# Optimization experiments

Measured on AMD Instinct MI355X. Metric: run time of the kernel, lower is better.

## Reference

```python
import jax, jax.numpy as jnp
import numpy as np

K_NN = 9  # kernel_size: neighbors per node (includes self, dist 0)


def knn_edges(feat):
    """feat: (B, C, N). Replicates DenseDilatedKnnGraph (dilation=1):
    L2-normalize over channels, dense pairwise sq-distance, top-k nearest."""
    nrm = jnp.sqrt(jnp.sum(feat * feat, axis=1, keepdims=True))
    xn = feat / jnp.maximum(nrm, 1e-12)            # F.normalize(dim=1)
    xt = jnp.swapaxes(xn, 1, 2)                    # (B, N, C)
    sq = jnp.sum(xt * xt, axis=-1)                 # (B, N)
    dist = sq[:, :, None] + sq[:, None, :] - 2.0 * jnp.einsum('bnc,bmc->bnm', xt, xt)
    _, nn_idx = jax.lax.top_k(-dist, K_NN)         # (B, N, k)
    center = jnp.broadcast_to(jnp.arange(nn_idx.shape[1], dtype=nn_idx.dtype)[None, :, None], nn_idx.shape)
    return nn_idx, center                          # (x_j sources, x_i targets)


def reference(x, W0, W1, bias):
    B, C, H, W = x.shape
    N = H * W
    NB = B * N
    feat = x.reshape(B, C, N)
    # KNN graph is built on detached features in the torch source
    x_j, x_i = knn_edges(jax.lax.stop_gradient(feat))
    E = B * N * K_NN
    # faithful to source: torch.linspace(0, B, steps=E, dtype=int64) batch offsets
    count = jnp.linspace(0.0, float(B), E).astype(jnp.int32)
    src = x_j.reshape(-1).astype(jnp.int32) + count * N
    dst = x_i.reshape(-1).astype(jnp.int32) + count * N
    valid = (src < NB) & (dst < NB)                # drop the out-of-range tail edge
    # flat_nodes: (B, C, H, W) -> (B*H*W, C), node id = b*HW + pixel
    nodes = jnp.swapaxes(feat, 1, 2).reshape(NB, C)
    # ChebConv K=2, sym norm, lambda_max=2: Tx0 = x, Tx1 = -(D^-1/2 A D^-1/2) x
    w = valid.astype(nodes.dtype)
    deg = jax.ops.segment_sum(w, src, num_segments=NB)
    dinv = jnp.where(deg > 0, jax.lax.rsqrt(jnp.maximum(deg, 1.0)), 0.0)
    norm = -(dinv[src] * w * dinv[dst])            # scaled-Laplacian edge weights
    msg = norm[:, None] * nodes[src]               # (E, C) gather + weight
    Tx1 = jax.ops.segment_sum(msg, dst, num_segments=NB)
    return nodes @ W0 + Tx1 @ W1 + bias


def setup_inputs() -> dict:
    key = jax.random.key(0)
    k1, k2, k3, k4 = jax.random.split(key, 4)
    B, C, H, W = 8, 48, 64, 64
    Cout = 48
    s = 1.0 / np.sqrt(C)
    return {
        'x': jax.random.normal(k1, (B, C, H, W), dtype=jnp.float32),
        'W0': jax.random.normal(k2, (C, Cout), dtype=jnp.float32) * s,
        'W1': jax.random.normal(k3, (C, Cout), dtype=jnp.float32) * s,
        'bias': jax.random.normal(k4, (Cout,), dtype=jnp.float32) * 0.01,
    }
```

## Files before the change

### kernel.cpp

```cpp
#include <hip/hip_runtime.h>

#define BATCH 8
#define CH    48
#define NPTS  4096
#define NBN   (BATCH*NPTS)
#define KNN   9
#define NCAND 12

typedef unsigned short u16;
typedef unsigned int   u32;
typedef unsigned long long u64;
typedef __bf16 bf16x8 __attribute__((ext_vector_type(8)));
typedef float  f32x4  __attribute__((ext_vector_type(4)));

__device__ __forceinline__ float bf2f(u16 v) { return __uint_as_float(((u32)v) << 16); }
__device__ __forceinline__ u16 f2bf(float f) {
  u32 u = __float_as_uint(f);
  u = (u + 0x7fffu + ((u >> 16) & 1u)) >> 16;
  return (u16)u;
}

#define MED3U(d, a, b, c) \
  asm("v_med3_u32 %0, %1, %2, %3" : "=v"(d) : "v"(a), "v"(b), "v"(c))
#define INS12(p0,p1,p2,p3,p4,p5,p6,p7,p8,p9,p10,p11,x) do { \
  MED3U(p11,p10,p11,x); MED3U(p10,p9,p10,x); MED3U(p9,p8,p9,x);  \
  MED3U(p8, p7, p8, x); MED3U(p7, p6,p7, x); MED3U(p6,p5,p6,x);  \
  MED3U(p5, p4, p5, x); MED3U(p4, p3,p4, x); MED3U(p3,p2,p3,x);  \
  MED3U(p2, p1, p2, x); MED3U(p1, p0,p1, x); p0 = min(p0, x);    \
} while (0)

__global__ __launch_bounds__(256)
void k_prep(const float* __restrict__ x, float* __restrict__ xraw,
            float* __restrict__ xn, float* __restrict__ csq,
            u16* __restrict__ Abuf, u16* __restrict__ Bbuf,
            int* __restrict__ deg) {
  int node = blockIdx.x * 256 + threadIdx.x;
  deg[node] = 0;
  int b = node >> 12, n = node & (NPTS - 1);
  const float* xb = x + (size_t)b * CH * NPTS;
  float f[CH];
#pragma unroll
  for (int c = 0; c < CH; ++c) f[c] = xb[(size_t)c * NPTS + n];
  float a0 = 0, a1 = 0, a2 = 0, a3 = 0;
#pragma unroll
  for (int k = 0; k < CH; k += 4) {
    a0 += f[k] * f[k]; a1 += f[k+1] * f[k+1];
    a2 += f[k+2] * f[k+2]; a3 += f[k+3] * f[k+3];
  }
  float nrm = fmaxf(sqrtf((a0 + a1) + (a2 + a3)), 1e-12f);
  float xv[CH];
#pragma unroll
  for (int c = 0; c < CH; ++c) xv[c] = f[c] / nrm;
  a0 = a1 = a2 = a3 = 0;
#pragma unroll
  for (int k = 0; k < CH; k += 4) {
    a0 += xv[k] * xv[k]; a1 += xv[k+1] * xv[k+1];
    a2 += xv[k+2] * xv[k+2]; a3 += xv[k+3] * xv[k+3];
  }
  float csqv = (a0 + a1) + (a2 + a3);
  csq[node] = csqv;
  float4* ro = (float4*)(xraw + (size_t)node * CH);
  float4* no = (float4*)(xn   + (size_t)node * CH);
#pragma unroll
  for (int i = 0; i < CH / 4; ++i) {
    ro[i] = make_float4(f[4*i], f[4*i+1], f[4*i+2], f[4*i+3]);
    no[i] = make_float4(xv[4*i], xv[4*i+1], xv[4*i+2], xv[4*i+3]);
  }
  u16 ah[64], al[64];
#pragma unroll
  for (int k = 0; k < CH; ++k) {
    float av = -2.0f * xv[k];
    u16 h = f2bf(av); ah[k] = h; al[k] = f2bf(av - bf2f(h));
  }
  { u16 h = f2bf(csqv); ah[48] = h; al[48] = f2bf(csqv - bf2f(h)); }
#pragma unroll
  for (int k = 49; k < 64; ++k) { ah[k] = 0; al[k] = 0; }
  u16* Bh = Bbuf + (size_t)node * 128;
#pragma unroll
  for (int k = 0; k < CH; ++k) {
    float bv = xv[k];
    u16 h = f2bf(bv); Bh[k] = h; Bh[64 + k] = f2bf(bv - bf2f(h));
  }
  Bh[48] = 0x3F80; Bh[64 + 48] = 0;
#pragma unroll
  for (int k = 49; k < 64; ++k) { Bh[k] = 0; Bh[64 + k] = 0; }
  u16* Ag = Abuf + (size_t)(node >> 4) * 2048 + (size_t)(node & 15) * 8;
#pragma unroll
  for (int v = 0; v < 4; ++v) {
    const u16* src = (v < 2) ? ah : al;
    int koff = (v & 1) * 32;
#pragma unroll
    for (int q = 0; q < 4; ++q) {
      uint4 pk;
      const u16* s = src + koff + q * 8;
      pk.x = (u32)s[0] | ((u32)s[1] << 16);
      pk.y = (u32)s[2] | ((u32)s[3] << 16);
      pk.z = (u32)s[4] | ((u32)s[5] << 16);
      pk.w = (u32)s[6] | ((u32)s[7] << 16);
      *(uint4*)(Ag + v * 512 + q * 128) = pk;
    }
  }
}

__global__ __launch_bounds__(256, 4)
void k_knn_m(const u16* __restrict__ Abuf, const u16* __restrict__ Bbuf,
             u32* __restrict__ candu) {
  int tid = threadIdx.x;
  int lane = tid & 63;
  int quad = lane >> 4, m16 = lane & 15;
  int panel = blockIdx.x * 4 + (tid >> 6);
  int row = panel * 16 + m16;
  int b4096 = row & ~(NPTS - 1);
  int quarter = blockIdx.y;
  int ct0 = quarter * 64;

  const __bf16* Bb = (const __bf16*)Bbuf + (size_t)row * 128;
  bf16x8 bh0 = *(const bf16x8*)(Bb + quad * 8);
  bf16x8 bh1 = *(const bf16x8*)(Bb + 32 + quad * 8);
  bf16x8 bl0 = *(const bf16x8*)(Bb + 64 + quad * 8);
  bf16x8 bl1 = *(const bf16x8*)(Bb + 96 + quad * 8);

  const __bf16* Ag = (const __bf16*)Abuf + (size_t)(b4096 >> 4) * 2048
                     + (size_t)lane * 8 + (size_t)ct0 * 2048;

  u32 s0=~0u,s1=~0u,s2=~0u,s3=~0u,s4=~0u,s5=~0u,
      s6=~0u,s7=~0u,s8=~0u,s9=~0u,s10=~0u,s11=~0u;

#define TILE_BODY(A0,A1,A2,A3,CT) do {                                      \
    f32x4 acc = {2.5f, 2.5f, 2.5f, 2.5f};                                   \
    acc = __builtin_amdgcn_mfma_f32_16x16x32_bf16(A0, bh0, acc, 0, 0, 0);   \
    acc = __builtin_amdgcn_mfma_f32_16x16x32_bf16(A1, bh1, acc, 0, 0, 0);   \
    acc = __builtin_amdgcn_mfma_f32_16x16x32_bf16(A0, bl0, acc, 0, 0, 0);   \
    acc = __builtin_amdgcn_mfma_f32_16x16x32_bf16(A1, bl1, acc, 0, 0, 0);   \
    acc = __builtin_amdgcn_mfma_f32_16x16x32_bf16(A2, bh0, acc, 0, 0, 0);   \
    acc = __builtin_amdgcn_mfma_f32_16x16x32_bf16(A3, bh1, acc, 0, 0, 0);   \
    u32 colb = ((u32)(CT) << 4) | ((u32)quad << 2);                         \
    _Pragma("unroll")                                                       \
    for (int r = 0; r < 4; ++r) {                                           \
      u32 u = __float_as_uint(acc[r]);                                      \
      u32 xx = (u & 0xFFFFF000u) | (colb | (u32)r);                         \
      INS12(s0,s1,s2,s3,s4,s5,s6,s7,s8,s9,s10,s11, xx);                     \
    }                                                                       \
  } while (0)

  bf16x8 a0 = *(const bf16x8*)(Ag);
  bf16x8 a1 = *(const bf16x8*)(Ag + 512);
  bf16x8 a2 = *(const bf16x8*)(Ag + 1024);
  bf16x8 a3 = *(const bf16x8*)(Ag + 1536);

  for (int t = 0; t < 64; t += 2) {
    const __bf16* apc = Ag + (size_t)(t + 1) * 2048;
    bf16x8 c0 = *(const bf16x8*)(apc);
    bf16x8 c1 = *(const bf16x8*)(apc + 512);
    bf16x8 c2 = *(const bf16x8*)(apc + 1024);
    bf16x8 c3 = *(const bf16x8*)(apc + 1536);

    TILE_BODY(a0, a1, a2, a3, ct0 + t);

    const __bf16* apn = Ag + (size_t)((t + 2 < 64) ? (t + 2) : 63) * 2048;
    a0 = *(const bf16x8*)(apn);
    a1 = *(const bf16x8*)(apn + 512);
    a2 = *(const bf16x8*)(apn + 1024);
    a3 = *(const bf16x8*)(apn + 1536);

    TILE_BODY(c0, c1, c2, c3, ct0 + t + 1);
  }
#undef TILE_BODY

  u32* o = candu + (((size_t)row * 4 + quarter) * 4 + quad) * NCAND;
  o[0]=s0; o[1]=s1; o[2]=s2; o[3]=s3; o[4]=s4; o[5]=s5;
  o[6]=s6; o[7]=s7; o[8]=s8; o[9]=s9; o[10]=s10; o[11]=s11;
}

__global__ __launch_bounds__(256, 4)
void k_reduce(const u32* __restrict__ candu, u32* __restrict__ cand12) {
  __shared__ u32 ls[64 * 4 * NCAND];
  int tid = threadIdx.x;
  int lr = tid >> 2, q = tid & 3;
  int row = blockIdx.x * 64 + lr;
  const u32* src = candu + (size_t)row * 192 + q * 48;
  u32 t0=~0u,t1=~0u,t2=~0u,t3=~0u,t4=~0u,t5=~0u,
      t6=~0u,t7=~0u,t8=~0u,t9=~0u,t10=~0u,t11=~0u;
  for (int s = 0; s < 48; ++s) {
    u32 x = src[s];
    INS12(t0,t1,t2,t3,t4,t5,t6,t7,t8,t9,t10,t11, x);
  }
  u32* lw = ls + (size_t)(lr * 4 + q) * NCAND;
  lw[0]=t0; lw[1]=t1; lw[2]=t2; lw[3]=t3; lw[4]=t4; lw[5]=t5;
  lw[6]=t6; lw[7]=t7; lw[8]=t8; lw[9]=t9; lw[10]=t10; lw[11]=t11;
  __syncthreads();
  if (q == 0) {
    u32 g0=~0u,g1=~0u,g2=~0u,g3=~0u,g4=~0u,g5=~0u,
        g6=~0u,g7=~0u,g8=~0u,g9=~0u,g10=~0u,g11=~0u;
    const u32* lsrc = ls + (size_t)lr * 48;
    for (int s = 0; s < 48; ++s) {
      u32 x = lsrc[s];
      INS12(g0,g1,g2,g3,g4,g5,g6,g7,g8,g9,g10,g11, x);
    }
    u32* o = cand12 + (size_t)row * NCAND;
    o[0]=(g0&0xFFFu); o[1]=(g1&0xFFFu); o[2]=(g2&0xFFFu);
    o[3]=(g3&0xFFFu); o[4]=(g4&0xFFFu); o[5]=(g5&0xFFFu);
    o[6]=(g6&0xFFFu); o[7]=(g7&0xFFFu); o[8]=(g8&0xFFFu);
    o[9]=(g9&0xFFFu); o[10]=(g10&0xFFFu); o[11]=(g11&0xFFFu);
  }
}

#define RR 16
__global__ __launch_bounds__(256, 4)
void k_rescore(const float* __restrict__ xn, const float* __restrict__ csq,
               const u32* __restrict__ cand12,
               u16* __restrict__ nn, int* __restrict__ deg) {
  __shared__ float dS[RR * NCAND];
  __shared__ int   iS[RR * NCAND];
  int tid = threadIdx.x;
  int lr = tid >> 4, q = tid & 15;
  int bi = blockIdx.x;
  int row = (bi & 7) * NPTS + (bi >> 3) * RR + lr;
  int b4096 = row & ~(NPTS - 1);
  const float* xnb = xn + (size_t)b4096 * CH;
  if (q < NCAND) {
    float rf[CH];
    const float4* p = (const float4*)(xn + (size_t)row * CH);
#pragma unroll
    for (int i = 0; i < CH / 4; ++i) {
      float4 v = p[i];
      rf[4*i] = v.x; rf[4*i+1] = v.y; rf[4*i+2] = v.z; rf[4*i+3] = v.w;
    }
    float sqn = csq[row];
    int c = (int)(cand12[(size_t)row * NCAND + q] & (NPTS - 1));
    const float4* cp = (const float4*)(xnb + (size_t)c * CH);
    float a0 = 0, a1 = 0, a2 = 0, a3 = 0;
#pragma unroll
    for (int i = 0; i < CH / 4; ++i) {
      float4 v = cp[i];
      a0 += rf[4*i]   * v.x; a1 += rf[4*i+1] * v.y;
      a2 += rf[4*i+2] * v.z; a3 += rf[4*i+3] * v.w;
    }
    float dist = (sqn + csq[b4096 + c]) - 2.0f * ((a0 + a1) + (a2 + a3));
    dS[lr * NCAND + q] = dist;
    iS[lr * NCAND + q] = c;
  }
  __syncthreads();
  if (q == 0) {
    float gd[KNN]; int gi[KNN];
#pragma unroll
    for (int j = 0; j < KNN; ++j) { gd[j] = 3.4e38f; gi[j] = 0x7fffffff; }
    for (int s = 0; s < NCAND; ++s) {
      float dc = dS[lr * NCAND + s]; int ic = iS[lr * NCAND + s];
      if (dc < gd[KNN - 1] || (dc == gd[KNN - 1] && ic < gi[KNN - 1])) {
        gd[KNN - 1] = dc; gi[KNN - 1] = ic;
#pragma unroll
        for (int k2 = KNN - 1; k2 > 0; --k2) {
          bool sw = (gd[k2] < gd[k2 - 1]) ||
                    (gd[k2] == gd[k2 - 1] && gi[k2] < gi[k2 - 1]);
          if (sw) {
            float td = gd[k2]; gd[k2] = gd[k2 - 1]; gd[k2 - 1] = td;
            int ti = gi[k2]; gi[k2] = gi[k2 - 1]; gi[k2 - 1] = ti;
          }
        }
      }
    }
    u16* o = nn + (size_t)row * KNN;
    int jmax = (row == NBN - 1) ? (KNN - 1) : KNN;
#pragma unroll
    for (int j = 0; j < KNN; ++j) o[j] = (u16)(gi[j] & (NPTS - 1));
    for (int j = 0; j < jmax; ++j)
      atomicAdd(&deg[b4096 + (gi[j] & (NPTS - 1))], 1);
  }
}

#define ONB 64
#define LPAD 52
__global__ __launch_bounds__(256)
void k_out_f(const float* __restrict__ xraw, const u16* __restrict__ nn,
             const int* __restrict__ deg,
             const float* __restrict__ W0, const float* __restrict__ W1,
             const float* __restrict__ bias, float* __restrict__ out) {
  __shared__ float w0[CH * CH], w1[CH * CH], bs[CH];
  __shared__ __align__(16) float fS[ONB * LPAD];
  __shared__ __align__(16) float txS[ONB * LPAD];
  __shared__ float dinvS[ONB];
  int tid = threadIdx.x;
  int bi = blockIdx.x;
  int n0 = (bi & 7) * NPTS + (bi >> 3) * ONB;
  int b12 = n0 & ~(NPTS - 1);
  for (int i = tid; i < CH * CH; i += 256) { w0[i] = W0[i]; w1[i] = W1[i]; }
  if (tid < CH) bs[tid] = bias[tid];
  for (int i = tid; i < ONB * 12; i += 256) {
    int ln = i / 12, f4 = i % 12;
    *(float4*)(fS + ln * LPAD + f4 * 4) =
        *(const float4*)(xraw + (size_t)(n0 + ln) * CH + f4 * 4);
  }
  if (tid < ONB) {
    int dg = deg[n0 + tid];
    dinvS[tid] = (dg > 0) ? (1.0f / sqrtf((float)dg)) : 0.0f;
  }
  __syncthreads();

  int ln = tid >> 2, p = tid & 3;
  int node = n0 + ln;
  float dn = dinvS[ln];
  const u16* nrow = nn + (size_t)node * KNN;
  bool full = (node != NBN - 1);
  float tx[12];
#pragma unroll
  for (int i = 0; i < 12; ++i) tx[i] = 0.f;
#pragma unroll
  for (int j = 0; j < KNN; ++j) {
    if (j < KNN - 1 || full) {
      int s = nrow[j] & (NPTS - 1);
      int dgs = deg[b12 + s];
      float ds = (dgs > 0) ? (1.0f / sqrtf((float)dgs)) : 0.0f;
      float w = -(ds * dn);
      const float4* pr = (const float4*)(xraw + (size_t)(b12 + s) * CH + p * 12);
#pragma unroll
      for (int q3 = 0; q3 < 3; ++q3) {
        float4 v = pr[q3];
        tx[q3*4]   += w * v.x; tx[q3*4+1] += w * v.y;
        tx[q3*4+2] += w * v.z; tx[q3*4+3] += w * v.w;
      }
    }
  }
#pragma unroll
  for (int q3 = 0; q3 < 3; ++q3)
    *(float4*)(txS + ln * LPAD + p * 12 + q3 * 4) =
        make_float4(tx[q3*4], tx[q3*4+1], tx[q3*4+2], tx[q3*4+3]);
  __syncthreads();

  float acc[12];
#pragma unroll
  for (int i = 0; i < 12; ++i) acc[i] = bs[p * 12 + i];
  const float* fr = fS + ln * LPAD;
  const float* tr = txS + ln * LPAD;
#pragma unroll
  for (int c = 0; c < CH; ++c) {
    float fc = fr[c];
    const float* wr = w0 + c * CH + p * 12;
#pragma unroll
    for (int i = 0; i < 12; ++i) acc[i] += fc * wr[i];
  }
#pragma unroll
  for (int c = 0; c < CH; ++c) {
    float tc = tr[c];
    const float* wr = w1 + c * CH + p * 12;
#pragma unroll
    for (int i = 0; i < 12; ++i) acc[i] += tc * wr[i];
  }
  float* op = out + (size_t)node * CH + p * 12;
#pragma unroll
  for (int q3 = 0; q3 < 3; ++q3)
    *(float4*)(op + q3 * 4) =
        make_float4(acc[q3*4], acc[q3*4+1], acc[q3*4+2], acc[q3*4+3]);
}

__global__ __launch_bounds__(256)
void k_zero(int* __restrict__ deg) { deg[blockIdx.x * 256 + threadIdx.x] = 0; }

__global__ __launch_bounds__(256)
void k_hist(const u16* __restrict__ nn, int* __restrict__ deg) {
  int node = blockIdx.x * 256 + threadIdx.x;
  int b12 = node & ~(NPTS - 1);
  int jmax = (node == NBN - 1) ? (KNN - 1) : KNN;
  for (int j = 0; j < jmax; ++j)
    atomicAdd(&deg[b12 + (nn[(size_t)node * KNN + j] & (NPTS - 1))], 1);
}

__global__ __launch_bounds__(256)
void k_dinv(const int* __restrict__ deg, float* __restrict__ dinv) {
  int i = blockIdx.x * 256 + threadIdx.x;
  int dg = deg[i];
  dinv[i] = (dg > 0) ? (1.0f / sqrtf((float)dg)) : 0.0f;
}

#define NQ    4
#define QCOLS (NPTS/NQ)
#define TCOLS 32
#define NTILES (QCOLS/TCOLS)
#define RPB   64

__global__ __launch_bounds__(256)
void k_knn_nb(const float* __restrict__ x, u16* __restrict__ nn) {
  __shared__ __align__(16) float tile[NQ * TCOLS * CH];
  __shared__ float nrmS[NQ * TCOLS];
  __shared__ float csq[NQ * TCOLS];
  int tid = threadIdx.x;
  int r0 = blockIdx.x * RPB;
  int b  = r0 >> 12;
  int q  = tid >> 6;
  int lr = tid & 63;
  int n  = (r0 + lr) & (NPTS - 1);
  const float* xb = x + (size_t)b * CH * NPTS;
  float rf[CH];
#pragma unroll
  for (int c = 0; c < CH; ++c) rf[c] = xb[(size_t)c * NPTS + n];
  float sqn;
  {
    float a0 = 0, a1 = 0, a2 = 0, a3 = 0;
#pragma unroll
    for (int k = 0; k < CH; k += 4) {
      a0 += rf[k] * rf[k]; a1 += rf[k+1] * rf[k+1];
      a2 += rf[k+2] * rf[k+2]; a3 += rf[k+3] * rf[k+3];
    }
    float nrm = fmaxf(sqrtf((a0 + a1) + (a2 + a3)), 1e-12f);
#pragma unroll
    for (int c = 0; c < CH; ++c) rf[c] = rf[c] / nrm;
    a0 = a1 = a2 = a3 = 0;
#pragma unroll
    for (int k = 0; k < CH; k += 4) {
      a0 += rf[k] * rf[k]; a1 += rf[k+1] * rf[k+1];
      a2 += rf[k+2] * rf[k+2]; a3 += rf[k+3] * rf[k+3];
    }
    sqn = (a0 + a1) + (a2 + a3);
  }
  float d[KNN]; int id[KNN];
#pragma unroll
  for (int j = 0; j < KNN; ++j) { d[j] = 3.4e38f; id[j] = 0x7fffffff; }
  for (int t = 0; t < NTILES; ++t) {
    __syncthreads();
#pragma unroll
    for (int qq = 0; qq < NQ; ++qq) {
      int colbase = qq * QCOLS + t * TCOLS;
      float* dst = tile + qq * TCOLS * CH;
#pragma unroll
      for (int it = 0; it < 6; ++it) {
        int i = it * 256 + tid;
        int c = i >> 5, p = i & 31;
        dst[p * CH + c] = xb[(size_t)c * NPTS + colbase + p];
      }
    }
    __syncthreads();
    if (tid < NQ * TCOLS) {
      const float* cp = tile + tid * CH;
      float a0 = 0, a1 = 0, a2 = 0, a3 = 0;
#pragma unroll
      for (int k = 0; k < CH; k += 4) {
        float4 v = *(const float4*)(cp + k);
        a0 += v.x * v.x; a1 += v.y * v.y; a2 += v.z * v.z; a3 += v.w * v.w;
      }
      nrmS[tid] = fmaxf(sqrtf((a0 + a1) + (a2 + a3)), 1e-12f);
    }
    __syncthreads();
    for (int i = tid; i < NQ * TCOLS * CH; i += 256)
      tile[i] = tile[i] / nrmS[i / CH];
    __syncthreads();
    if (tid < NQ * TCOLS) {
      const float* cp = tile + tid * CH;
      float a0 = 0, a1 = 0, a2 = 0, a3 = 0;
#pragma unroll
      for (int k = 0; k < CH; k += 4) {
        float4 v = *(const float4*)(cp + k);
        a0 += v.x * v.x; a1 += v.y * v.y; a2 += v.z * v.z; a3 += v.w * v.w;
      }
      csq[tid] = (a0 + a1) + (a2 + a3);
    }
    __syncthreads();
    int cbase = q * QCOLS + t * TCOLS;
    const float* tq = tile + q * TCOLS * CH;
    for (int cc = 0; cc < TCOLS; ++cc) {
      const float* cp = tq + cc * CH;
      float a0 = 0, a1 = 0, a2 = 0, a3 = 0;
#pragma unroll
      for (int k = 0; k < CH; k += 4) {
        float4 v = *(const float4*)(cp + k);
        a0 += rf[k] * v.x; a1 += rf[k+1] * v.y;
        a2 += rf[k+2] * v.z; a3 += rf[k+3] * v.w;
      }
      float dist = (sqn + csq[q * TCOLS + cc]) - 2.0f * ((a0 + a1) + (a2 + a3));
      if (dist < d[KNN - 1]) {
        d[KNN - 1] = dist; id[KNN - 1] = cbase + cc;
#pragma unroll
        for (int k2 = KNN - 1; k2 > 0; --k2) {
          if (d[k2] < d[k2 - 1]) {
            float td = d[k2]; d[k2] = d[k2 - 1]; d[k2 - 1] = td;
            int ti = id[k2]; id[k2] = id[k2 - 1]; id[k2 - 1] = ti;
          }
        }
      }
    }
  }
  __syncthreads();
  float* md = tile;
  int*   mi = (int*)(tile + 256 * KNN);
#pragma unroll
  for (int j = 0; j < KNN; ++j) { md[tid * KNN + j] = d[j]; mi[tid * KNN + j] = id[j]; }
  __syncthreads();
  if (tid < RPB) {
    float fd[KNN]; int fi[KNN];
#pragma unroll
    for (int j = 0; j < KNN; ++j) { fd[j] = 3.4e38f; fi[j] = 0x7fffffff; }
    for (int qq = 0; qq < NQ; ++qq) {
      int s = qq * RPB + tid;
      for (int j = 0; j < KNN; ++j) {
        float dc = md[s * KNN + j]; int ic = mi[s * KNN + j];
        if (dc < fd[KNN - 1]) {
          fd[KNN - 1] = dc; fi[KNN - 1] = ic;
#pragma unroll
          for (int k2 = KNN - 1; k2 > 0; --k2) {
            if (fd[k2] < fd[k2 - 1]) {
              float td = fd[k2]; fd[k2] = fd[k2 - 1]; fd[k2 - 1] = td;
              int ti = fi[k2]; fi[k2] = fi[k2 - 1]; fi[k2 - 1] = ti;
            }
          }
        }
      }
    }
    u16* o = nn + (size_t)(r0 + tid) * KNN;
#pragma unroll
    for (int j = 0; j < KNN; ++j) o[j] = (u16)(fi[j] & (NPTS - 1));
  }
}

__global__ __launch_bounds__(256)
void k_out_nb(const float* __restrict__ x, const u16* __restrict__ nn,
              const float* __restrict__ dinv,
              const float* __restrict__ W0, const float* __restrict__ W1,
              const float* __restrict__ bias, float* __restrict__ out) {
  __shared__ float w0[CH * CH], w1[CH * CH], bs[CH];
  for (int i = threadIdx.x; i < CH * CH; i += 256) { w0[i] = W0[i]; w1[i] = W1[i]; }
  if (threadIdx.x < CH) bs[threadIdx.x] = bias[threadIdx.x];
  __syncthreads();
  int node = blockIdx.x * 256 + threadIdx.x;
  int b = node >> 12, n = node & (NPTS - 1);
  const float* xb = x + (size_t)b * CH * NPTS;
  float f[CH], acc[CH], tx[CH];
#pragma unroll
  for (int c = 0; c < CH; ++c) f[c] = xb[(size_t)c * NPTS + n];
#pragma unroll
  for (int o = 0; o < CH; ++o) acc[o] = bs[o];
#pragma unroll
  for (int c = 0; c < CH; ++c) {
    float fc = f[c];
    const float* wr = w0 + c * CH;
#pragma unroll
    for (int o = 0; o < CH; ++o) acc[o] += fc * wr[o];
  }
#pragma unroll
  for (int c = 0; c < CH; ++c) tx[c] = 0.f;
  float dn = dinv[node];
  int jmax = (node == NBN - 1) ? (KNN - 1) : KNN;
  for (int j = 0; j < jmax; ++j) {
    int s = nn[(size_t)node * KNN + j] & (NPTS - 1);
    float w = -(dinv[(b << 12) + s] * dn);
#pragma unroll
    for (int c = 0; c < CH; ++c) tx[c] += w * xb[(size_t)c * NPTS + s];
  }
#pragma unroll
  for (int c = 0; c < CH; ++c) {
    float tc = tx[c];
    const float* wr = w1 + c * CH;
#pragma unroll
    for (int o = 0; o < CH; ++o) acc[o] += tc * wr[o];
  }
  float4* op = (float4*)(out + (size_t)node * CH);
#pragma unroll
  for (int i = 0; i < CH / 4; ++i)
    op[i] = make_float4(acc[4*i], acc[4*i+1], acc[4*i+2], acc[4*i+3]);
}

extern "C" void kernel_launch(void* const* d_in, const int* in_sizes, int n_in,
                              void* d_out, int out_size, void* d_ws, size_t ws_size,
                              hipStream_t stream) {
  const float* x    = (const float*)d_in[0];
  const float* W0   = (const float*)d_in[1];
  const float* W1   = (const float*)d_in[2];
  const float* bias = (const float*)d_in[3];
  float* out = (float*)d_out;
  char* w = (char*)d_ws;

  const size_t SZ_XN   = (size_t)NBN * CH * 4;
  const size_t SZ_XRAW = (size_t)NBN * CH * 4;
  const size_t SZ_CSQ  = (size_t)NBN * 4;
  const size_t SZ_NN   = (size_t)NBN * KNN * 2;
  const size_t SZ_DEG  = (size_t)NBN * 4;
  const size_t SZ_AB   = (size_t)NBN * 128 * 2;
  const size_t SZ_CU   = (size_t)NBN * 16 * NCAND * 4;
  const size_t SZ_C12  = (size_t)NBN * NCAND * 4;
  const size_t needF = SZ_XN + SZ_XRAW + SZ_CSQ + SZ_NN + SZ_DEG
                     + 2 * SZ_AB + SZ_CU + SZ_C12;

  if (ws_size >= needF) {
    size_t off = 0;
    float* xn   = (float*)(w + off); off += SZ_XN;
    float* xraw = (float*)(w + off); off += SZ_XRAW;
    float* csq  = (float*)(w + off); off += SZ_CSQ;
    u16*   nn   = (u16*)  (w + off); off += SZ_NN;
    int*   deg  = (int*)  (w + off); off += SZ_DEG;
    u16*   Abuf = (u16*)  (w + off); off += SZ_AB;
    u16*   Bbuf = (u16*)  (w + off); off += SZ_AB;
    u32*   candu= (u32*)  (w + off); off += SZ_CU;
    u32*   cand12=(u32*)  (w + off);
    k_prep    <<<NBN / 256, 256, 0, stream>>>(x, xraw, xn, csq, Abuf, Bbuf, deg);
    k_knn_m   <<<dim3(NBN / 64, 4), 256, 0, stream>>>(Abuf, Bbuf, candu);
    k_reduce  <<<NBN / 64, 256, 0, stream>>>(candu, cand12);
    k_rescore <<<NBN / RR, 256, 0, stream>>>(xn, csq, cand12, nn, deg);
    k_out_f   <<<NBN / ONB, 256, 0, stream>>>(xraw, nn, deg, W0, W1, bias, out);
  } else {
    u16*   nn   = (u16*)w;
    int*   deg  = (int*)(w + SZ_NN);
    float* dinv = (float*)(w + SZ_NN + SZ_DEG);
    k_knn_nb <<<NBN / RPB, 256, 0, stream>>>(x, nn);
    k_zero   <<<NBN / 256, 256, 0, stream>>>(deg);
    k_hist   <<<NBN / 256, 256, 0, stream>>>(nn, deg);
    k_dinv   <<<NBN / 256, 256, 0, stream>>>(deg, dinv);
    k_out_nb <<<NBN / 256, 256, 0, stream>>>(x, nn, dinv, W0, W1, bias, out);
  }
}
```

Before: 225.5 us.

## Stage KNN A-tiles through LDS with async global_load_lds double buffering

The KNN distance kernel used to have every wave load the shared A column tile from global memory into registers. Now the four waves of a block each copy a quarter of the tile into a double-buffered LDS array using global_load_lds, then read it back from LDS. It also software-pipelines the loop so the top-12 filter of the previous tile runs alongside the MFMAs of the next tile, and raises the launch-bounds occupancy hint from 4 to 6. The aim is to cut redundant global or L2 traffic and hide load latency, at the cost of a block barrier on every tile and more register pressure.

```diff
diff --git a/kernel.cpp b/kernel.cpp
--- a/kernel.cpp
+++ b/kernel.cpp
@@ -28,6 +28,12 @@
   MED3U(p5, p4, p5, x); MED3U(p4, p3,p4, x); MED3U(p3,p2,p3,x);  \
   MED3U(p2, p1, p2, x); MED3U(p1, p0,p1, x); p0 = min(p0, x);    \
 } while (0)
+
+__device__ __forceinline__ void stage_q(const u16* g, u16* l) {
+  __builtin_amdgcn_global_load_lds(
+      (const __attribute__((address_space(1))) void*)g,
+      (__attribute__((address_space(3))) void*)l, 16, 0, 0);
+}
 
 __global__ __launch_bounds__(256)
 void k_prep(const float* __restrict__ x, float* __restrict__ xraw,
@@ -102,13 +108,15 @@
   }
 }
 
-__global__ __launch_bounds__(256, 4)
+__global__ __launch_bounds__(256, 6)
 void k_knn_m(const u16* __restrict__ Abuf, const u16* __restrict__ Bbuf,
              u32* __restrict__ candu) {
+  __shared__ __align__(16) u16 As[2][2048];
   int tid = threadIdx.x;
   int lane = tid & 63;
+  int wv = tid >> 6;
   int quad = lane >> 4, m16 = lane & 15;
-  int panel = blockIdx.x * 4 + (tid >> 6);
+  int panel = blockIdx.x * 4 + wv;
   int row = panel * 16 + m16;
   int b4096 = row & ~(NPTS - 1);
   int quarter = blockIdx.y;
@@ -120,52 +128,69 @@
   bf16x8 bl0 = *(const bf16x8*)(Bb + 64 + quad * 8);
   bf16x8 bl1 = *(const bf16x8*)(Bb + 96 + quad * 8);
 
-  const __bf16* Ag = (const __bf16*)Abuf + (size_t)(b4096 >> 4) * 2048
-                     + (size_t)lane * 8 + (size_t)ct0 * 2048;
+  const u16* gs = Abuf + ((size_t)(b4096 >> 4) + ct0) * 2048
+                  + wv * 512 + lane * 8;
 
   u32 s0=~0u,s1=~0u,s2=~0u,s3=~0u,s4=~0u,s5=~0u,
       s6=~0u,s7=~0u,s8=~0u,s9=~0u,s10=~0u,s11=~0u;
 
-#define TILE_BODY(A0,A1,A2,A3,CT) do {                                      \
-    f32x4 acc = {2.5f, 2.5f, 2.5f, 2.5f};                                   \
-    acc = __builtin_amdgcn_mfma_f32_16x16x32_bf16(A0, bh0, acc, 0, 0, 0);   \
-    acc = __builtin_amdgcn_mfma_f32_16x16x32_bf16(A1, bh1, acc, 0, 0, 0);   \
-    acc = __builtin_amdgcn_mfma_f32_16x16x32_bf16(A0, bl0, acc, 0, 0, 0);   \
-    acc = __builtin_amdgcn_mfma_f32_16x16x32_bf16(A1, bl1, acc, 0, 0, 0);   \
-    acc = __builtin_amdgcn_mfma_f32_16x16x32_bf16(A2, bh0, acc, 0, 0, 0);   \
-    acc = __builtin_amdgcn_mfma_f32_16x16x32_bf16(A3, bh1, acc, 0, 0, 0);   \
-    u32 colb = ((u32)(CT) << 4) | ((u32)quad << 2);                         \
+#define LDA(BUF, A0,A1,A2,A3) do {                                          \
+    const u16* _p = &As[BUF][lane * 8];                                     \
+    A0 = *(const bf16x8*)(_p);                                              \
+    A1 = *(const bf16x8*)(_p + 512);                                        \
+    A2 = *(const bf16x8*)(_p + 1024);                                       \
+    A3 = *(const bf16x8*)(_p + 1536);                                       \
+  } while (0)
+#define MFMA6(ACC, A0,A1,A2,A3) do {                                        \
+    ACC = (f32x4){2.5f, 2.5f, 2.5f, 2.5f};                                  \
+    ACC = __builtin_amdgcn_mfma_f32_16x16x32_bf16(A0, bh0, ACC, 0, 0, 0);   \
+    ACC = __builtin_amdgcn_mfma_f32_16x16x32_bf16(A1, bh1, ACC, 0, 0, 0);   \
+    ACC = __builtin_amdgcn_mfma_f32_16x16x32_bf16(A0, bl0, ACC, 0, 0, 0);   \
+    ACC = __builtin_amdgcn_mfma_f32_16x16x32_bf16(A1, bl1, ACC, 0, 0, 0);   \
+    ACC = __builtin_amdgcn_mfma_f32_16x16x32_bf16(A2, bh0, ACC, 0, 0, 0);   \
+    ACC = __builtin_amdgcn_mfma_f32_16x16x32_bf16(A3, bh1, ACC, 0, 0, 0);   \
+  } while (0)
+#define FILTER(ACC, CT) do {                                                \
+    u32 _colb = ((u32)(CT) << 4) | ((u32)quad << 2);                        \
     _Pragma("unroll")                                                       \
-    for (int r = 0; r < 4; ++r) {                                           \
-      u32 u = __float_as_uint(acc[r]);                                      \
-      u32 xx = (u & 0xFFFFF000u) | (colb | (u32)r);                         \
-      INS12(s0,s1,s2,s3,s4,s5,s6,s7,s8,s9,s10,s11, xx);                     \
+    for (int _r = 0; _r < 4; ++_r) {                                        \
+      u32 _u = __float_as_uint((ACC)[_r]);                                  \
+      u32 _x = (_u & 0xFFFFF000u) | (_colb | (u32)_r);                      \
+      INS12(s0,s1,s2,s3,s4,s5,s6,s7,s8,s9,s10,s11, _x);                     \
     }                                                                       \
   } while (0)
 
-  bf16x8 a0 = *(const bf16x8*)(Ag);
-  bf16x8 a1 = *(const bf16x8*)(Ag + 512);
-  bf16x8 a2 = *(const bf16x8*)(Ag + 1024);
-  bf16x8 a3 = *(const bf16x8*)(Ag + 1536);
-
-  for (int t = 0; t < 64; t += 2) {
-    const __bf16* apc = Ag + (size_t)(t + 1) * 2048;
-    bf16x8 c0 = *(const bf16x8*)(apc);
-    bf16x8 c1 = *(const bf16x8*)(apc + 512);
-    bf16x8 c2 = *(const bf16x8*)(apc + 1024);
-    bf16x8 c3 = *(const bf16x8*)(apc + 1536);
-
-    TILE_BODY(a0, a1, a2, a3, ct0 + t);
-
-    const __bf16* apn = Ag + (size_t)((t + 2 < 64) ? (t + 2) : 63) * 2048;
-    a0 = *(const bf16x8*)(apn);
-    a1 = *(const bf16x8*)(apn + 512);
-    a2 = *(const bf16x8*)(apn + 1024);
-    a3 = *(const bf16x8*)(apn + 1536);
-
-    TILE_BODY(c0, c1, c2, c3, ct0 + t + 1);
-  }
-#undef TILE_BODY
+  f32x4 accA, accB;
+  bf16x8 a0, a1, a2, a3;
+
+  stage_q(gs, &As[0][wv * 512]);
+  __syncthreads();
+
+  LDA(0, a0, a1, a2, a3);
+  stage_q(gs + (size_t)1 * 2048, &As[1][wv * 512]);
+  MFMA6(accA, a0, a1, a2, a3);
+  __syncthreads();
+
+  for (int i = 0; i < 31; ++i) {
+    int t = 2 * i + 1;
+    LDA(1, a0, a1, a2, a3);
+    stage_q(gs + (size_t)(t + 1) * 2048, &As[0][wv * 512]);
+    FILTER(accA, ct0 + t - 1);
+    MFMA6(accB, a0, a1, a2, a3);
+    __syncthreads();
+    LDA(0, a0, a1, a2, a3);
+    stage_q(gs + (size_t)(t + 2) * 2048, &As[1][wv * 512]);
+    FILTER(accB, ct0 + t);
+    MFMA6(accA, a0, a1, a2, a3);
+    __syncthreads();
+  }
+  LDA(1, a0, a1, a2, a3);
+  FILTER(accA, ct0 + 62);
+  MFMA6(accB, a0, a1, a2, a3);
+  FILTER(accB, ct0 + 63);
+#undef LDA
+#undef MFMA6
+#undef FILTER
 
   u32* o = candu + (((size_t)row * 4 + quarter) * 4 + quad) * NCAND;
   o[0]=s0; o[1]=s1; o[2]=s2; o[3]=s3; o[4]=s4; o[5]=s5;
```

New measurement: 213.9 us. 1.05x faster.
